# Optimization experiments

Measured on AMD Instinct MI355X. Metric: run time of the kernel, lower is better.

Reference implementation:

```python
import jax, jax.numpy as jnp
import numpy as np

N_NODES = 50000
N_EDGES = 800000
D_IN = 64
H1 = 64
H2 = 64
N_CLASSES = 10
N_GRAPHS = 500


def setup_inputs() -> dict:
    key = jax.random.key(0)
    ks = jax.random.split(key, 9)
    x = jax.random.normal(ks[0], (N_NODES, D_IN), dtype=jnp.float32)
    edge_index = jax.random.randint(ks[1], (2, N_EDGES), 0, N_NODES, dtype=jnp.int64)
    batch = jnp.sort(jax.random.randint(ks[2], (N_NODES,), 0, N_GRAPHS, dtype=jnp.int64))
    # Linear params (Kaiming-uniform-ish scale)
    def lin(k, fin, fout):
        kw, kb = jax.random.split(k)
        s = 1.0 / np.sqrt(fin)
        W = jax.random.uniform(kw, (fin, fout), minval=-s, maxval=s, dtype=jnp.float32)
        b = jax.random.uniform(kb, (fout,), minval=-s, maxval=s, dtype=jnp.float32)
        return W, b
    W1, b1 = lin(ks[3], D_IN, H1)
    W2, b2 = lin(ks[4], H1, H2)
    W3, b3 = lin(ks[5], H2, N_CLASSES)
    return {"x": x, "edge_index": edge_index, "batch": batch,
            "W1": W1, "b1": b1, "W2": W2, "b2": b2, "W3": W3, "b3": b3}


def _gin_conv(h, src, dst, W, b, eps=0.0):
    # sum aggregation of neighbor messages: msg[i] = sum_{(j->i)} h[j]
    agg = jax.ops.segment_sum(h[src], dst, num_segments=N_NODES)
    return ((1.0 + eps) * h + agg) @ W + b


def reference(x, edge_index, batch, W1, b1, W2, b2, W3, b3):
    src, dst = edge_index[0], edge_index[1]
    h = jax.nn.relu(_gin_conv(x, src, dst, W1, b1))
    h = jax.nn.relu(_gin_conv(h, src, dst, W2, b2))
    # global mean pool over graphs
    sums = jax.ops.segment_sum(h, batch, num_segments=N_GRAPHS)
    cnt = jax.ops.segment_sum(jnp.ones((N_NODES,), dtype=h.dtype), batch, num_segments=N_GRAPHS)
    pooled = sums / jnp.maximum(cnt, 1.0)[:, None]
    return pooled @ W3 + b3
```

## Files before the change

kernel.cpp:

```cpp
#include <hip/hip_runtime.h>
#include <hip/hip_bf16.h>
#include <hip/hip_fp16.h>


#define N_FEAT 64
#define CHUNK 4096
#define CAP 6144

typedef _Float16 f16;
typedef _Float16 half8 __attribute__((ext_vector_type(8)));
typedef float float4v __attribute__((ext_vector_type(4)));

__device__ inline f16 cvt_f16(float v) { return (f16)v; }
__device__ inline f16 cvt_f16(f16 v) { return v; }

template <typename TIN>
__device__ __forceinline__ void gemm_body(const TIN* __restrict__ X, const float* __restrict__ W,
                                          f16* __restrict__ Z, int nrows, int bidx, char* smemc) {
    f16 (*sX)[72] = (f16 (*)[72])smemc;
    f16 (*sWT)[72] = (f16 (*)[72])(smemc + 64 * 72 * sizeof(f16));
    int t = threadIdx.x;
    int base = bidx * 64;
    for (int idx = t; idx < 4096; idx += 256) {
        int k = idx >> 6, n = idx & 63;
        sWT[n][k] = (f16)W[idx];
    }
    for (int idx = t; idx < 4096; idx += 256) {
        int r = idx >> 6, c = idx & 63;
        int row = base + r;
        sX[r][c] = (row < nrows) ? cvt_f16(X[(size_t)row * 64 + c]) : (f16)0.f;
    }
    __syncthreads();
    int wave = t >> 6;
    int lane = t & 63;
    int quad = lane >> 4;
    int m16 = lane & 15;
    half8 a0 = *(const half8*)&sX[wave * 16 + m16][quad * 8];
    half8 a1 = *(const half8*)&sX[wave * 16 + m16][32 + quad * 8];
    float4v acc[4];
#pragma unroll
    for (int C = 0; C < 4; ++C) {
        half8 b0 = *(const half8*)&sWT[C * 16 + m16][quad * 8];
        half8 b1 = *(const half8*)&sWT[C * 16 + m16][32 + quad * 8];
        float4v d = {0.f, 0.f, 0.f, 0.f};
        d = __builtin_amdgcn_mfma_f32_16x16x32_f16(a0, b0, d, 0, 0, 0);
        d = __builtin_amdgcn_mfma_f32_16x16x32_f16(a1, b1, d, 0, 0, 0);
        acc[C] = d;
    }
#pragma unroll
    for (int reg = 0; reg < 4; ++reg) {
        int row = base + wave * 16 + quad * 4 + reg;
        if (row < nrows) {
#pragma unroll
            for (int C = 0; C < 4; ++C)
                Z[(size_t)row * 64 + C * 16 + m16] = (f16)acc[C][reg];
        }
    }
}

__global__ __launch_bounds__(256) void bucket_scatter(const int* __restrict__ src, const int* __restrict__ dst,
                               int* __restrict__ ccur, int* __restrict__ staging, int E) {
    __shared__ int epack[CHUNK];
    __shared__ int ebkt[CHUNK];
    __shared__ int hist[256];
    __shared__ int base[256];
    int t = threadIdx.x;
    int begin = blockIdx.x * CHUNK;
    int cnt = min(CHUNK, E - begin);
    hist[t] = 0;
    __syncthreads();
    for (int i = t; i < cnt; i += 256) {
        int d = dst[begin + i];
        int s = src[begin + i];
        epack[i] = (s & 0xFFFF) | ((d & 255) << 16);
        ebkt[i] = d >> 8;
        atomicAdd(&hist[d >> 8], 1);
    }
    __syncthreads();
    int h = hist[t];
    if (h > 0) base[t] = atomicAdd(&ccur[t], h);
    hist[t] = 0;
    __syncthreads();
    for (int i = t; i < cnt; i += 256) {
        int b = ebkt[i];
        int off = base[b] + atomicAdd(&hist[b], 1);
        if (off < CAP) staging[(size_t)b * CAP + off] = epack[i];
    }
}

__device__ __forceinline__ void finalize_body(const int* __restrict__ staging, const int* __restrict__ ccur,
                                              int2* __restrict__ rowse, int* __restrict__ col, int N,
                                              int b, char* smemc) {
    int* edges = (int*)smemc;
    int* hist = edges + CAP;
    int* scan = hist + 256;
    int* cur = scan + 256;
    int t = threadIdx.x;
    int cnt = min(ccur[b], CAP);
    int sbase = b * CAP;
    hist[t] = 0;
    __syncthreads();
    for (int i = t; i < cnt; i += 256) {
        int e = staging[(size_t)sbase + i];
        edges[i] = e;
        atomicAdd(&hist[(e >> 16) & 255], 1);
    }
    __syncthreads();
    int v = hist[t];
    scan[t] = v;
    __syncthreads();
    for (int off = 1; off < 256; off <<= 1) {
        int u = (t >= off) ? scan[t - off] : 0;
        __syncthreads();
        scan[t] += u;
        __syncthreads();
    }
    int excl = scan[t] - v;
    cur[t] = excl;
    int node = b * 256 + t;
    if (node < N) rowse[node] = make_int2(sbase + excl, sbase + excl + v);
    __syncthreads();
    for (int i = t; i < cnt; i += 256) {
        int e = edges[i];
        int pos = sbase + atomicAdd(&cur[(e >> 16) & 255], 1);
        col[pos] = e & 0xFFFF;
    }
}

__global__ __launch_bounds__(256) void fused_finalize_gemm(
        const int* __restrict__ staging, const int* __restrict__ ccur,
        int2* __restrict__ rowse, int* __restrict__ col, int N,
        const float* __restrict__ X, const float* __restrict__ W,
        f16* __restrict__ Z, int nrows, int nbf) {
    __shared__ __align__(16) char smem[(CAP + 768) * 4];
    if ((int)blockIdx.x < nbf)
        finalize_body(staging, ccur, rowse, col, N, blockIdx.x, smem);
    else
        gemm_body<float>(X, W, Z, nrows, blockIdx.x - nbf, smem);
}

__global__ __launch_bounds__(512) void gather_gemm(
        const f16* __restrict__ Z, const int2* __restrict__ rowse,
        const int* __restrict__ col, const float* __restrict__ bias,
        const float* __restrict__ W2, f16* __restrict__ Z2, int n) {
    __shared__ f16 sH[32][72];
    __shared__ f16 sWT[64][72];
    int t = threadIdx.x;
    for (int idx = t; idx < 4096; idx += 512) {
        int k = idx >> 6, nn = idx & 63;
        sWT[nn][k] = (f16)W2[idx];
    }
    int w = t >> 6;
    int lane = t & 63;
    int e = lane >> 3, c = lane & 7;
    int base = blockIdx.x * 32;
    const float4v* Z4 = reinterpret_cast<const float4v*>(Z);
    const float4* B4 = reinterpret_cast<const float4*>(bias);
#pragma unroll
    for (int q = 0; q < 4; ++q) {
        int node = base + w * 4 + q;
        bool valid = node < n;
        int lo = 0, hi = 0;
        if (valid) { int2 se = rowse[node]; lo = se.x; hi = se.y; }
        float acc[8] = {0.f, 0.f, 0.f, 0.f, 0.f, 0.f, 0.f, 0.f};
        int idx4[4];
#pragma unroll
        for (int i = 0; i < 4; ++i) {
            int j = lo + e + i * 8;
            idx4[i] = (j < hi) ? col[j] : -1;
        }
#pragma unroll
        for (int i = 0; i < 4; ++i) {
            if (idx4[i] >= 0) {
                float4v r = Z4[(size_t)idx4[i] * 8 + c];
                half8 hv = *(half8*)&r;
#pragma unroll
                for (int k = 0; k < 8; ++k) acc[k] += (float)hv[k];
            }
        }
        for (int j = lo + 32 + e; j < hi; j += 8) {
            float4v r = Z4[(size_t)col[j] * 8 + c];
            half8 hv = *(half8*)&r;
#pragma unroll
            for (int k = 0; k < 8; ++k) acc[k] += (float)hv[k];
        }
#pragma unroll
        for (int k = 0; k < 8; ++k) {
            acc[k] += __shfl_xor(acc[k], 8);
            acc[k] += __shfl_xor(acc[k], 16);
            acc[k] += __shfl_xor(acc[k], 32);
        }
        if (e == 0) {
            half8 o;
            if (valid) {
                float4v sr = Z4[(size_t)node * 8 + c];
                half8 sv = *(half8*)&sr;
                float4 b0 = B4[c * 2];
                float4 b1 = B4[c * 2 + 1];
                float bb[8] = {b0.x, b0.y, b0.z, b0.w, b1.x, b1.y, b1.z, b1.w};
#pragma unroll
                for (int k = 0; k < 8; ++k)
                    o[k] = (f16)fmaxf((float)sv[k] + acc[k] + bb[k], 0.f);
            } else {
#pragma unroll
                for (int k = 0; k < 8; ++k) o[k] = (f16)0.f;
            }
            *(half8*)&sH[w * 4 + q][c * 8] = o;
        }
    }
    __syncthreads();
    int quad = lane >> 4;
    int m16 = lane & 15;
    int mrow = (w >> 2) * 16;
    int ncol = (w & 3) * 16;
    half8 a0 = *(const half8*)&sH[mrow + m16][quad * 8];
    half8 a1 = *(const half8*)&sH[mrow + m16][32 + quad * 8];
    half8 b0 = *(const half8*)&sWT[ncol + m16][quad * 8];
    half8 b1 = *(const half8*)&sWT[ncol + m16][32 + quad * 8];
    float4v d = {0.f, 0.f, 0.f, 0.f};
    d = __builtin_amdgcn_mfma_f32_16x16x32_f16(a0, b0, d, 0, 0, 0);
    d = __builtin_amdgcn_mfma_f32_16x16x32_f16(a1, b1, d, 0, 0, 0);
#pragma unroll
    for (int reg = 0; reg < 4; ++reg) {
        int row = base + mrow + quad * 4 + reg;
        if (row < n)
            Z2[(size_t)row * 64 + ncol + m16] = (f16)d[reg];
    }
}

template <int POOL>
__global__ __launch_bounds__(256) void gather_relu2(
        const f16* __restrict__ Z, const int2* __restrict__ rowse,
        const int* __restrict__ col, const float* __restrict__ bias,
        f16* __restrict__ H, float* __restrict__ sums,
        const int* __restrict__ batch, int n) {
    __shared__ float sh[4][64];
    __shared__ int gid[4];
    int w = threadIdx.x >> 6;
    int node = (int)(blockIdx.x * 4 + w);
    int lane = threadIdx.x & 63;
    int e = lane >> 3, c = lane & 7;
    bool valid = node < n;
    int lo = 0, hi = 0;
    if (valid) { int2 se = rowse[node]; lo = se.x; hi = se.y; }
    const float4v* Z4 = reinterpret_cast<const float4v*>(Z);
    float acc[8] = {0.f, 0.f, 0.f, 0.f, 0.f, 0.f, 0.f, 0.f};
    int idx[4];
#pragma unroll
    for (int i = 0; i < 4; ++i) {
        int j = lo + e + i * 8;
        idx[i] = (j < hi) ? col[j] : -1;
    }
#pragma unroll
    for (int i = 0; i < 4; ++i) {
        if (idx[i] >= 0) {
            float4v r = Z4[(size_t)idx[i] * 8 + c];
            half8 hv = *(half8*)&r;
#pragma unroll
            for (int k = 0; k < 8; ++k) acc[k] += (float)hv[k];
        }
    }
    for (int j = lo + 32 + e; j < hi; j += 8) {
        float4v r = Z4[(size_t)col[j] * 8 + c];
        half8 hv = *(half8*)&r;
#pragma unroll
        for (int k = 0; k < 8; ++k) acc[k] += (float)hv[k];
    }
#pragma unroll
    for (int k = 0; k < 8; ++k) {
        acc[k] += __shfl_xor(acc[k], 8);
        acc[k] += __shfl_xor(acc[k], 16);
        acc[k] += __shfl_xor(acc[k], 32);
    }
    if (POOL) {
        if (lane == 0) gid[w] = valid ? batch[node] : -1;
    }
    if (valid && e == 0) {
        float4v sr = Z4[(size_t)node * 8 + c];
        half8 sv = *(half8*)&sr;
        const float4* B4 = reinterpret_cast<const float4*>(bias);
        float4 b0 = B4[c * 2];
        float4 b1 = B4[c * 2 + 1];
        float bb[8] = {b0.x, b0.y, b0.z, b0.w, b1.x, b1.y, b1.z, b1.w};
        float h[8];
#pragma unroll
        for (int k = 0; k < 8; ++k) h[k] = fmaxf((float)sv[k] + acc[k] + bb[k], 0.f);
        if (!POOL) {
            half8 o;
#pragma unroll
            for (int k = 0; k < 8; ++k) o[k] = (f16)h[k];
            reinterpret_cast<half8*>(H)[(size_t)node * 8 + c] = o;
        } else {
#pragma unroll
            for (int k = 0; k < 8; ++k) sh[w][c * 8 + k] = h[k];
        }
    }
    if (POOL) {
        __syncthreads();
        if (w == 0) {
            int cg = gid[0];
            float run = 0.f;
#pragma unroll
            for (int q = 0; q < 4; ++q) {
                int g = gid[q];
                if (g < 0) break;
                if (g != cg) {
                    atomicAdd(&sums[cg * 64 + lane], run);
                    run = 0.f;
                    cg = g;
                }
                run += sh[q][lane];
            }
            if (cg >= 0) atomicAdd(&sums[cg * 64 + lane], run);
        }
    }
}

__global__ __launch_bounds__(64) void head_kernel(
        const float* __restrict__ sums, const int* __restrict__ batch,
        const float* __restrict__ W3, const float* __restrict__ b3,
        float* __restrict__ out, int n, int ncls) {
    int g = blockIdx.x;
    __shared__ float row[64];
    __shared__ int bnd[2];
    int t = threadIdx.x;
    if (t < 2) {
        int target = g + t;
        int lo = 0, hi = n;
        while (lo < hi) { int m = (lo + hi) >> 1; if (batch[m] < target) lo = m + 1; else hi = m; }
        bnd[t] = lo;
    }
    __syncthreads();
    float cnt = fmaxf((float)(bnd[1] - bnd[0]), 1.0f);
    row[t] = sums[g * 64 + t] / cnt;
    __syncthreads();
    if (t < ncls) {
        float o = b3[t];
#pragma unroll
        for (int k = 0; k < 64; ++k) o += row[k] * W3[k * ncls + t];
        out[g * ncls + t] = o;
    }
}

extern "C" void kernel_launch(void* const* d_in, const int* in_sizes, int n_in,
                              void* d_out, int out_size, void* d_ws, size_t ws_size,
                              hipStream_t stream) {
    const float* x     = (const float*)d_in[0];
    const int*   ei    = (const int*)d_in[1];
    const int*   batch = (const int*)d_in[2];
    const float* W1    = (const float*)d_in[3];
    const float* b1    = (const float*)d_in[4];
    const float* W2    = (const float*)d_in[5];
    const float* b2    = (const float*)d_in[6];
    const float* W3    = (const float*)d_in[7];
    const float* b3    = (const float*)d_in[8];
    float* out = (float*)d_out;

    const int N = in_sizes[0] / N_FEAT;
    const int E = in_sizes[1] / 2;
    const int NCLS = 10;
    const int G = out_size / NCLS;
    const int* src = ei;
    const int* dst = ei + E;
    const int nb = (N + 255) / 256;

    int*   staging = (int*)d_ws;
    int2*  rowse   = (int2*)(staging + (size_t)nb * CAP);
    int*   col     = (int*)(rowse + N);
    int*   ccur    = col + (size_t)nb * CAP;
    float* sums    = (float*)(ccur + 256);
    f16*   zbuf    = (f16*)(sums + (size_t)G * 64);
    f16*   z2buf   = zbuf + (size_t)N * 64;

    const int gemmGrid = (N + 63) / 64;
    const int gg2Grid  = (N + 31) / 32;
    const int gatherGrid = (N + 3) / 4;
    const int scatGrid = (E + CHUNK - 1) / CHUNK;

    hipMemsetAsync(ccur, 0, (256 + (size_t)G * 64) * sizeof(int), stream);
    bucket_scatter<<<scatGrid, 256, 0, stream>>>(src, dst, ccur, staging, E);

    fused_finalize_gemm<<<nb + gemmGrid, 256, 0, stream>>>(
        staging, ccur, rowse, col, N, x, W1, zbuf, N, nb);

    gather_gemm<<<gg2Grid, 512, 0, stream>>>(zbuf, rowse, col, b1, W2, z2buf, N);

    gather_relu2<1><<<gatherGrid, 256, 0, stream>>>(z2buf, rowse, col, b2, nullptr, sums, batch, N);

    head_kernel<<<G, 64, 0, stream>>>(sums, batch, W3, b3, out, N, NCLS);
}
```

Baseline: 169.4 us.

## Fuse edge scatter with first GEMM, shrink buckets, and store columns as u16

The edge bucketing scatter now runs inside the same launch as the layer-1 GEMM, and finalize becomes its own kernel. The aim is to overlap the scatter work with the dense GEMM. Buckets shrink from 256 to 128 nodes, with smaller chunks and per-bucket capacity, which cuts LDS use and gives finalize more parallelism. Column indices are stored as 16-bit values to halve index traffic in the gather kernels. The risks are more scatter blocks issuing global atomics, a capacity overflow that silently drops edges, and source indices truncated to 16 bits (a 50000-node graph fits).

Result: slower. 183.6 us (+8.4%).

```diff
diff --git a/kernel.cpp b/kernel.cpp
--- a/kernel.cpp
+++ b/kernel.cpp
@@ -4,12 +4,16 @@
 
 
 #define N_FEAT 64
-#define CHUNK 4096
-#define CAP 6144
+#define CHUNK 1024
+#define BSH 7
+#define BNODES 128
+#define NBKT_MAX 400
+#define CAP2 2816
 
 typedef _Float16 f16;
 typedef _Float16 half8 __attribute__((ext_vector_type(8)));
 typedef float float4v __attribute__((ext_vector_type(4)));
+typedef unsigned short u16;
 
 __device__ inline f16 cvt_f16(float v) { return (f16)v; }
 __device__ inline f16 cvt_f16(f16 v) { return v; }
@@ -58,90 +62,95 @@
     }
 }
 
-__global__ __launch_bounds__(256) void bucket_scatter(const int* __restrict__ src, const int* __restrict__ dst,
-                               int* __restrict__ ccur, int* __restrict__ staging, int E) {
-    __shared__ int epack[CHUNK];
-    __shared__ int ebkt[CHUNK];
-    __shared__ int hist[256];
-    __shared__ int base[256];
+__device__ __forceinline__ void scatter_body(const int* __restrict__ src, const int* __restrict__ dst,
+                                             int* __restrict__ ccur, int* __restrict__ staging,
+                                             int E, int nbkt, int bidx, char* smemc) {
+    int* epack = (int*)smemc;
+    int* ebkt  = epack + CHUNK;
+    int* hist  = ebkt + CHUNK;
+    int* base  = hist + NBKT_MAX;
     int t = threadIdx.x;
-    int begin = blockIdx.x * CHUNK;
+    int begin = bidx * CHUNK;
     int cnt = min(CHUNK, E - begin);
-    hist[t] = 0;
+    for (int i = t; i < nbkt; i += 256) hist[i] = 0;
     __syncthreads();
     for (int i = t; i < cnt; i += 256) {
         int d = dst[begin + i];
         int s = src[begin + i];
-        epack[i] = (s & 0xFFFF) | ((d & 255) << 16);
-        ebkt[i] = d >> 8;
-        atomicAdd(&hist[d >> 8], 1);
-    }
-    __syncthreads();
-    int h = hist[t];
-    if (h > 0) base[t] = atomicAdd(&ccur[t], h);
-    hist[t] = 0;
+        epack[i] = (s & 0xFFFF) | ((d & (BNODES - 1)) << 16);
+        ebkt[i] = d >> BSH;
+        atomicAdd(&hist[d >> BSH], 1);
+    }
+    __syncthreads();
+    for (int i = t; i < nbkt; i += 256) {
+        int h = hist[i];
+        if (h > 0) base[i] = atomicAdd(&ccur[i], h);
+        hist[i] = 0;
+    }
     __syncthreads();
     for (int i = t; i < cnt; i += 256) {
         int b = ebkt[i];
         int off = base[b] + atomicAdd(&hist[b], 1);
-        if (off < CAP) staging[(size_t)b * CAP + off] = epack[i];
-    }
-}
-
-__device__ __forceinline__ void finalize_body(const int* __restrict__ staging, const int* __restrict__ ccur,
-                                              int2* __restrict__ rowse, int* __restrict__ col, int N,
-                                              int b, char* smemc) {
-    int* edges = (int*)smemc;
-    int* hist = edges + CAP;
-    int* scan = hist + 256;
-    int* cur = scan + 256;
-    int t = threadIdx.x;
-    int cnt = min(ccur[b], CAP);
-    int sbase = b * CAP;
-    hist[t] = 0;
+        if (off < CAP2) staging[(size_t)b * CAP2 + off] = epack[i];
+    }
+}
+
+__global__ __launch_bounds__(256) void fused_scatter_gemm(
+        const int* __restrict__ src, const int* __restrict__ dst,
+        int* __restrict__ ccur, int* __restrict__ staging, int E, int nbkt,
+        const float* __restrict__ X, const float* __restrict__ W,
+        f16* __restrict__ Z, int nrows, int nsb) {
+    __shared__ __align__(16) char smem[2 * 64 * 72 * sizeof(f16)];
+    if ((int)blockIdx.x < nsb)
+        scatter_body(src, dst, ccur, staging, E, nbkt, blockIdx.x, smem);
+    else
+        gemm_body<float>(X, W, Z, nrows, blockIdx.x - nsb, smem);
+}
+
+__global__ __launch_bounds__(256) void bucket_finalize(
+        const int* __restrict__ staging, const int* __restrict__ ccur,
+        int2* __restrict__ rowse, u16* __restrict__ col, int N) {
+    __shared__ int edges[CAP2];
+    __shared__ int hist[BNODES];
+    __shared__ int scan[BNODES];
+    __shared__ int cur[BNODES];
+    int b = blockIdx.x, t = threadIdx.x;
+    int cnt = min(ccur[b], CAP2);
+    int sbase = b * CAP2;
+    if (t < BNODES) hist[t] = 0;
     __syncthreads();
     for (int i = t; i < cnt; i += 256) {
         int e = staging[(size_t)sbase + i];
         edges[i] = e;
-        atomicAdd(&hist[(e >> 16) & 255], 1);
-    }
-    __syncthreads();
-    int v = hist[t];
-    scan[t] = v;
-    __syncthreads();
-    for (int off = 1; off < 256; off <<= 1) {
-        int u = (t >= off) ? scan[t - off] : 0;
+        atomicAdd(&hist[(e >> 16) & (BNODES - 1)], 1);
+    }
+    __syncthreads();
+    int v = (t < BNODES) ? hist[t] : 0;
+    if (t < BNODES) scan[t] = v;
+    __syncthreads();
+    for (int off = 1; off < BNODES; off <<= 1) {
+        int u = (t >= off && t < BNODES) ? scan[t - off] : 0;
         __syncthreads();
-        scan[t] += u;
+        if (t < BNODES) scan[t] += u;
         __syncthreads();
     }
-    int excl = scan[t] - v;
-    cur[t] = excl;
-    int node = b * 256 + t;
-    if (node < N) rowse[node] = make_int2(sbase + excl, sbase + excl + v);
+    if (t < BNODES) {
+        int excl = scan[t] - v;
+        cur[t] = excl;
+        int node = b * BNODES + t;
+        if (node < N) rowse[node] = make_int2(sbase + excl, sbase + excl + v);
+    }
     __syncthreads();
     for (int i = t; i < cnt; i += 256) {
         int e = edges[i];
-        int pos = sbase + atomicAdd(&cur[(e >> 16) & 255], 1);
-        col[pos] = e & 0xFFFF;
-    }
-}
-
-__global__ __launch_bounds__(256) void fused_finalize_gemm(
-        const int* __restrict__ staging, const int* __restrict__ ccur,
-        int2* __restrict__ rowse, int* __restrict__ col, int N,
-        const float* __restrict__ X, const float* __restrict__ W,
-        f16* __restrict__ Z, int nrows, int nbf) {
-    __shared__ __align__(16) char smem[(CAP + 768) * 4];
-    if ((int)blockIdx.x < nbf)
-        finalize_body(staging, ccur, rowse, col, N, blockIdx.x, smem);
-    else
-        gemm_body<float>(X, W, Z, nrows, blockIdx.x - nbf, smem);
+        int pos = sbase + atomicAdd(&cur[(e >> 16) & (BNODES - 1)], 1);
+        col[pos] = (u16)(e & 0xFFFF);
+    }
 }
 
 __global__ __launch_bounds__(512) void gather_gemm(
         const f16* __restrict__ Z, const int2* __restrict__ rowse,
-        const int* __restrict__ col, const float* __restrict__ bias,
+        const u16* __restrict__ col, const float* __restrict__ bias,
         const float* __restrict__ W2, f16* __restrict__ Z2, int n) {
     __shared__ f16 sH[32][72];
     __shared__ f16 sWT[64][72];
@@ -167,7 +176,7 @@
 #pragma unroll
         for (int i = 0; i < 4; ++i) {
             int j = lo + e + i * 8;
-            idx4[i] = (j < hi) ? col[j] : -1;
+            idx4[i] = (j < hi) ? (int)col[j] : -1;
         }
 #pragma unroll
         for (int i = 0; i < 4; ++i) {
@@ -179,7 +188,7 @@
             }
         }
         for (int j = lo + 32 + e; j < hi; j += 8) {
-            float4v r = Z4[(size_t)col[j] * 8 + c];
+            float4v r = Z4[(size_t)(int)col[j] * 8 + c];
             half8 hv = *(half8*)&r;
 #pragma unroll
             for (int k = 0; k < 8; ++k) acc[k] += (float)hv[k];
@@ -228,12 +237,10 @@
     }
 }
 
-template <int POOL>
-__global__ __launch_bounds__(256) void gather_relu2(
+__global__ __launch_bounds__(256) void gather_pool(
         const f16* __restrict__ Z, const int2* __restrict__ rowse,
-        const int* __restrict__ col, const float* __restrict__ bias,
-        f16* __restrict__ H, float* __restrict__ sums,
-        const int* __restrict__ batch, int n) {
+        const u16* __restrict__ col, const float* __restrict__ bias,
+        float* __restrict__ sums, const int* __restrict__ batch, int n) {
     __shared__ float sh[4][64];
     __shared__ int gid[4];
     int w = threadIdx.x >> 6;
@@ -249,7 +256,7 @@
 #pragma unroll
     for (int i = 0; i < 4; ++i) {
         int j = lo + e + i * 8;
-        idx[i] = (j < hi) ? col[j] : -1;
+        idx[i] = (j < hi) ? (int)col[j] : -1;
     }
 #pragma unroll
     for (int i = 0; i < 4; ++i) {
@@ -261,7 +268,7 @@
         }
     }
     for (int j = lo + 32 + e; j < hi; j += 8) {
-        float4v r = Z4[(size_t)col[j] * 8 + c];
+        float4v r = Z4[(size_t)(int)col[j] * 8 + c];
         half8 hv = *(half8*)&r;
 #pragma unroll
         for (int k = 0; k < 8; ++k) acc[k] += (float)hv[k];
@@ -272,9 +279,7 @@
         acc[k] += __shfl_xor(acc[k], 16);
         acc[k] += __shfl_xor(acc[k], 32);
     }
-    if (POOL) {
-        if (lane == 0) gid[w] = valid ? batch[node] : -1;
-    }
+    if (lane == 0) gid[w] = valid ? batch[node] : -1;
     if (valid && e == 0) {
         float4v sr = Z4[(size_t)node * 8 + c];
         half8 sv = *(half8*)&sr;
@@ -282,37 +287,26 @@
         float4 b0 = B4[c * 2];
         float4 b1 = B4[c * 2 + 1];
         float bb[8] = {b0.x, b0.y, b0.z, b0.w, b1.x, b1.y, b1.z, b1.w};
-        float h[8];
-#pragma unroll
-        for (int k = 0; k < 8; ++k) h[k] = fmaxf((float)sv[k] + acc[k] + bb[k], 0.f);
-        if (!POOL) {
-            half8 o;
-#pragma unroll
-            for (int k = 0; k < 8; ++k) o[k] = (f16)h[k];
-            reinterpret_cast<half8*>(H)[(size_t)node * 8 + c] = o;
-        } else {
-#pragma unroll
-            for (int k = 0; k < 8; ++k) sh[w][c * 8 + k] = h[k];
-        }
-    }
-    if (POOL) {
-        __syncthreads();
-        if (w == 0) {
-            int cg = gid[0];
-            float run = 0.f;
-#pragma unroll
-            for (int q = 0; q < 4; ++q) {
-                int g = gid[q];
-                if (g < 0) break;
-                if (g != cg) {
-                    atomicAdd(&sums[cg * 64 + lane], run);
-                    run = 0.f;
-                    cg = g;
-                }
-                run += sh[q][lane];
+#pragma unroll
+        for (int k = 0; k < 8; ++k)
+            sh[w][c * 8 + k] = fmaxf((float)sv[k] + acc[k] + bb[k], 0.f);
+    }
+    __syncthreads();
+    if (w == 0) {
+        int cg = gid[0];
+        float run = 0.f;
+#pragma unroll
+        for (int q = 0; q < 4; ++q) {
+            int g = gid[q];
+            if (g < 0) break;
+            if (g != cg) {
+                atomicAdd(&sums[cg * 64 + lane], run);
+                run = 0.f;
+                cg = g;
             }
-            if (cg >= 0) atomicAdd(&sums[cg * 64 + lane], run);
-        }
+            run += sh[q][lane];
+        }
+        if (cg >= 0) atomicAdd(&sums[cg * 64 + lane], run);
     }
 }
 
@@ -362,30 +356,32 @@
     const int G = out_size / NCLS;
     const int* src = ei;
     const int* dst = ei + E;
-    const int nb = (N + 255) / 256;
+    const int nbkt = (N + BNODES - 1) / BNODES;
 
     int*   staging = (int*)d_ws;
-    int2*  rowse   = (int2*)(staging + (size_t)nb * CAP);
-    int*   col     = (int*)(rowse + N);
-    int*   ccur    = col + (size_t)nb * CAP;
-    float* sums    = (float*)(ccur + 256);
+    int2*  rowse   = (int2*)(staging + (size_t)nbkt * CAP2);
+    u16*   col     = (u16*)(rowse + N);
+    size_t colInts = ((size_t)nbkt * CAP2 * 2 + 15) / 16 * 4;
+    int*   ccur    = (int*)(rowse + N) + colInts;
+    float* sums    = (float*)(ccur + NBKT_MAX);
     f16*   zbuf    = (f16*)(sums + (size_t)G * 64);
     f16*   z2buf   = zbuf + (size_t)N * 64;
 
     const int gemmGrid = (N + 63) / 64;
+    const int nsb = (E + CHUNK - 1) / CHUNK;
     const int gg2Grid  = (N + 31) / 32;
     const int gatherGrid = (N + 3) / 4;
-    const int scatGrid = (E + CHUNK - 1) / CHUNK;
-
-    hipMemsetAsync(ccur, 0, (256 + (size_t)G * 64) * sizeof(int), stream);
-    bucket_scatter<<<scatGrid, 256, 0, stream>>>(src, dst, ccur, staging, E);
-
-    fused_finalize_gemm<<<nb + gemmGrid, 256, 0, stream>>>(
-        staging, ccur, rowse, col, N, x, W1, zbuf, N, nb);
+
+    hipMemsetAsync(ccur, 0, (NBKT_MAX + (size_t)G * 64) * sizeof(int), stream);
+
+    fused_scatter_gemm<<<nsb + gemmGrid, 256, 0, stream>>>(
+        src, dst, ccur, staging, E, nbkt, x, W1, zbuf, N, nsb);
+
+    bucket_finalize<<<nbkt, 256, 0, stream>>>(staging, ccur, rowse, col, N);
 
     gather_gemm<<<gg2Grid, 512, 0, stream>>>(zbuf, rowse, col, b1, W2, z2buf, N);
 
-    gather_relu2<1><<<gatherGrid, 256, 0, stream>>>(z2buf, rowse, col, b2, nullptr, sums, batch, N);
+    gather_pool<<<gatherGrid, 256, 0, stream>>>(z2buf, rowse, col, b2, sums, batch, N);
 
     head_kernel<<<G, 64, 0, stream>>>(sums, batch, W3, b3, out, N, NCLS);
 }
```
